# Kernel tuning notes

Measured on AMD Instinct MI355X. Metric: run time of the kernel, lower is better.

The kernel has to match this reference:

```python
import jax, jax.numpy as jnp
import numpy as np

N = 50000      # nodes
E = 800000     # edges (avg degree 16)
IN_DIM = 128
H = 4          # attention heads
D = 32         # hidden dim per head
NEG_SLOPE = 0.2


def setup_inputs() -> dict:
    key = jax.random.key(0)
    ks = jax.random.split(key, 9)
    x = jax.random.normal(ks[0], (N, IN_DIM), dtype=jnp.float32)
    src = jax.random.randint(ks[1], (E,), 0, N, dtype=jnp.int64)
    dst = jax.random.randint(ks[2], (E,), 0, N, dtype=jnp.int64)
    # layer 0: IN_DIM -> H*D ; layer 1: H*D -> H*D
    s0 = 1.0 / np.sqrt(IN_DIM)
    s1 = 1.0 / np.sqrt(H * D)
    W1 = jax.random.normal(ks[3], (H * D, IN_DIM), dtype=jnp.float32) * s0
    al1 = jax.random.normal(ks[4], (1, H, D), dtype=jnp.float32) * s1
    ar1 = jax.random.normal(ks[5], (1, H, D), dtype=jnp.float32) * s1
    W2 = jax.random.normal(ks[6], (H * D, H * D), dtype=jnp.float32) * s1
    al2 = jax.random.normal(ks[7], (1, H, D), dtype=jnp.float32) * s1
    ar2 = jax.random.normal(ks[8], (1, H, D), dtype=jnp.float32) * s1
    return {"x": x, "src": src, "dst": dst, "W1": W1, "al1": al1, "ar1": ar1,
            "W2": W2, "al2": al2, "ar2": ar2}


def gat_conv(h, src, dst, W, al, ar):
    """DGL-style GATConv. h: [N, F_in] -> [N, H, D], with ELU activation."""
    feat = (h @ W.T).reshape(N, H, D)                 # [N,H,D]
    el = jnp.sum(feat * al, axis=-1)                  # [N,H] a_l . Wh
    er = jnp.sum(feat * ar, axis=-1)                  # [N,H] a_r . Wh
    e = jax.nn.leaky_relu(el[src] + er[dst], NEG_SLOPE)  # [E,H]
    # numerically stable edge softmax over incoming edges of each dst node
    m = jax.ops.segment_max(e, dst, num_segments=N)   # [N,H]
    ee = jnp.exp(e - m[dst])                          # [E,H]
    denom = jax.ops.segment_sum(ee, dst, num_segments=N)  # [N,H]
    alpha = ee / denom[dst]                           # [E,H]
    msg = feat[src] * alpha[..., None]                # [E,H,D]
    out = jax.ops.segment_sum(msg, dst, num_segments=N)   # [N,H,D]
    return jax.nn.elu(out)


def reference(x, src, dst, W1, al1, ar1, W2, al2, ar2):
    h = gat_conv(x, src, dst, W1, al1, ar1).reshape(N, H * D)  # flatten(1)
    h = gat_conv(h, src, dst, W2, al2, ar2)                    # [N,H,D]
    return jnp.mean(h, axis=1)                                 # [N,D]
```

## Files before the change

### kernel.cpp

```cpp
#include <hip/hip_runtime.h>
#include <cmath>

#define HEADS 4
#define FDIM 128
#define NEG 0.2f

typedef __attribute__((ext_vector_type(8))) __bf16 bf16x8;
typedef __attribute__((ext_vector_type(8))) _Float16 h16x8;
typedef __attribute__((ext_vector_type(4))) float f32x4;

__global__ __launch_bounds__(256) void prep_kernel(
    const float* __restrict__ W1, const float* __restrict__ al1,
    const float* __restrict__ ar1,
    const float* __restrict__ W2, const float* __restrict__ al2,
    const float* __restrict__ ar2,
    __bf16* __restrict__ wf1, __bf16* __restrict__ wext1,
    __bf16* __restrict__ wf2, __bf16* __restrict__ wext2)
{
    const int b = blockIdx.x, tid = threadIdx.x;
    if (b < 256) {
        const float* W = (b < 128) ? W1 : W2;
        __bf16* wf = (b < 128) ? wf1 : wf2;
        int idx = (b & 127) * 256 + tid;
        int j = idx & 7;
        int r = idx >> 3;
        int c = r & 15; r >>= 4;
        int t = r & 7;  r >>= 3;
        int kq = r & 15;
        int hl = r >> 4;
        float v = W[(t * 16 + c) * 128 + kq * 8 + j];
        __bf16 hi = (__bf16)v;
        wf[idx] = (hl == 0) ? hi : (__bf16)(v - (float)hi);
    } else {
        const float* W  = (b == 256) ? W1 : W2;
        const float* al = (b == 256) ? al1 : al2;
        const float* ar = (b == 256) ? ar1 : ar2;
        __bf16* wext = (b == 256) ? wext1 : wext2;
        __shared__ float val[1024];
        #pragma unroll
        for (int ch = 0; ch < 4; ++ch) {
            int idx = ch * 256 + tid;
            int c = idx >> 7, k = idx & 127;
            int h = c & 3;
            const float* a = (c < 4) ? al : ar;
            float s = 0.f;
            for (int d = 0; d < 32; ++d)
                s += a[h * 32 + d] * W[(h * 32 + d) * 128 + k];
            val[c * 128 + k] = s;
        }
        __syncthreads();
        #pragma unroll
        for (int ch = 0; ch < 16; ++ch) {
            int idx = tid * 16 + ch;
            int j = idx & 7;
            int r = idx >> 3;
            int c = r & 15; r >>= 4;
            int kq = r & 15;
            int hl = r >> 4;
            float v = (c < 8) ? val[c * 128 + kq * 8 + j] : 0.f;
            __bf16 hi = (__bf16)v;
            wext[idx] = (hl == 0) ? hi : (__bf16)(v - (float)hi);
        }
    }
}

__global__ __launch_bounds__(256) void gemm_mfma_kernel(
    const float* __restrict__ X, const bf16x8* __restrict__ wf,
    const bf16x8* __restrict__ wext,
    _Float16* __restrict__ featH,
    float* __restrict__ el, float* __restrict__ er,
    int nnodes, int ntiles)
{
    __shared__ bf16x8 lw[4096];
    const int tid = threadIdx.x;
    for (int i = tid; i < 4096; i += 256) lw[i] = wf[i];
    __syncthreads();

    const int wave = tid >> 6, lane = tid & 63;
    const int l15 = lane & 15, quad = lane >> 4;

    int tile = blockIdx.x;
    float4 xr[8], xn[8];

    auto loadX = [&](int tl, float4* dst) {
        int nodeA = tl * 64 + wave * 16 + l15;
        bool v = nodeA < nnodes;
        const float4* xp = (const float4*)(X + (size_t)nodeA * 128);
        #pragma unroll
        for (int ks = 0; ks < 4; ++ks) {
            dst[2 * ks]     = v ? xp[ks * 8 + quad * 2]     : make_float4(0.f, 0.f, 0.f, 0.f);
            dst[2 * ks + 1] = v ? xp[ks * 8 + quad * 2 + 1] : make_float4(0.f, 0.f, 0.f, 0.f);
        }
    };

    loadX(tile, xr);
    while (true) {
        int next = tile + gridDim.x;
        if (next < ntiles) loadX(next, xn);

        f32x4 acc[9];
        #pragma unroll
        for (int t = 0; t < 9; ++t) acc[t] = (f32x4){0.f, 0.f, 0.f, 0.f};

        #pragma unroll
        for (int ks = 0; ks < 4; ++ks) {
            float xa[8] = {xr[2 * ks].x, xr[2 * ks].y, xr[2 * ks].z, xr[2 * ks].w,
                           xr[2 * ks + 1].x, xr[2 * ks + 1].y, xr[2 * ks + 1].z, xr[2 * ks + 1].w};
            bf16x8 ahi, alo;
            #pragma unroll
            for (int j = 0; j < 8; ++j) {
                __bf16 h = (__bf16)xa[j];
                ahi[j] = h;
                alo[j] = (__bf16)(xa[j] - (float)h);
            }
            const int kq = ks * 4 + quad;

            {
                bf16x8 bh = wext[(kq) * 16 + l15];
                bf16x8 bl = wext[(16 + kq) * 16 + l15];
                acc[8] = __builtin_amdgcn_mfma_f32_16x16x32_bf16(ahi, bh, acc[8], 0, 0, 0);
                acc[8] = __builtin_amdgcn_mfma_f32_16x16x32_bf16(alo, bh, acc[8], 0, 0, 0);
                acc[8] = __builtin_amdgcn_mfma_f32_16x16x32_bf16(ahi, bl, acc[8], 0, 0, 0);
            }
            #pragma unroll
            for (int t = 0; t < 8; ++t) {
                bf16x8 bh = lw[(kq * 8 + t) * 16 + l15];
                bf16x8 bl = lw[((16 + kq) * 8 + t) * 16 + l15];
                acc[t] = __builtin_amdgcn_mfma_f32_16x16x32_bf16(ahi, bh, acc[t], 0, 0, 0);
                acc[t] = __builtin_amdgcn_mfma_f32_16x16x32_bf16(alo, bh, acc[t], 0, 0, 0);
                acc[t] = __builtin_amdgcn_mfma_f32_16x16x32_bf16(ahi, bl, acc[t], 0, 0, 0);
            }
        }

        const int nodeC = tile * 64 + wave * 16 + quad * 4;
        #pragma unroll
        for (int r = 0; r < 4; ++r) {
            int gn = nodeC + r;
            if (gn < nnodes) {
                #pragma unroll
                for (int t = 0; t < 8; ++t)
                    featH[(size_t)gn * 128 + t * 16 + l15] = (_Float16)acc[t][r];
            }
        }
        if (l15 < 8) {
            #pragma unroll
            for (int r = 0; r < 4; ++r) {
                int gn = nodeC + r;
                if (gn < nnodes) {
                    if (l15 < 4) el[gn * HEADS + l15] = acc[8][r];
                    else         er[gn * HEADS + (l15 - 4)] = acc[8][r];
                }
            }
        }

        if (next >= ntiles) break;
        #pragma unroll
        for (int i = 0; i < 8; ++i) xr[i] = xn[i];
        tile = next;
    }
}

__global__ __launch_bounds__(256) void hist_kernel(
    const int* __restrict__ dst, int* __restrict__ counts,
    int* __restrict__ rank, int nedges)
{
    int i0 = (blockIdx.x * 256 + threadIdx.x) * 4;
    if (i0 + 3 < nedges) {
        int4 d = *(const int4*)&dst[i0];
        int4 r;
        r.x = atomicAdd(&counts[d.x], 1);
        r.y = atomicAdd(&counts[d.y], 1);
        r.z = atomicAdd(&counts[d.z], 1);
        r.w = atomicAdd(&counts[d.w], 1);
        *(int4*)&rank[i0] = r;
    } else {
        for (int i = i0; i < nedges; ++i)
            rank[i] = atomicAdd(&counts[dst[i]], 1);
    }
}

__global__ __launch_bounds__(256) void scan1_kernel(
    const int* __restrict__ counts, int* __restrict__ offsets,
    int* __restrict__ bsums, int n)
{
    __shared__ int wsums[4];
    const int tid = threadIdx.x, lane = tid & 63, w = tid >> 6;
    const int i = blockIdx.x * 1024 + tid * 4;

    int4 v = make_int4(0, 0, 0, 0);
    if (i + 3 < n) v = *(const int4*)&counts[i];
    else {
        if (i < n)     v.x = counts[i];
        if (i + 1 < n) v.y = counts[i + 1];
        if (i + 2 < n) v.z = counts[i + 2];
    }
    int s0 = v.x, s1 = s0 + v.y, s2 = s1 + v.z, s3 = s2 + v.w;

    int x = s3;
    #pragma unroll
    for (int off = 1; off < 64; off <<= 1) {
        int t = __shfl_up(x, off, 64);
        if (lane >= off) x += t;
    }
    if (lane == 63) wsums[w] = x;
    __syncthreads();
    int wbase = 0;
    #pragma unroll
    for (int k = 0; k < 4; ++k) if (k < w) wbase += wsums[k];

    int tbase = wbase + x - s3;
    if (i < n)     offsets[i]     = tbase;
    if (i + 1 < n) offsets[i + 1] = tbase + s0;
    if (i + 2 < n) offsets[i + 2] = tbase + s1;
    if (i + 3 < n) offsets[i + 3] = tbase + s2;
    if (tid == 255) bsums[blockIdx.x] = wbase + x;
}

__global__ __launch_bounds__(64) void scan2_kernel(int* __restrict__ bsums, int nb)
{
    const int lane = threadIdx.x;
    int run = 0;
    for (int base = 0; base < nb; base += 64) {
        int i = base + lane;
        int v = (i < nb) ? bsums[i] : 0;
        int x = v;
        #pragma unroll
        for (int off = 1; off < 64; off <<= 1) {
            int t = __shfl_up(x, off, 64);
            if (lane >= off) x += t;
        }
        if (i < nb) bsums[i] = run + x - v;
        run += __shfl(x, 63, 64);
    }
}

__global__ __launch_bounds__(256) void scan3_kernel(
    int* __restrict__ offsets, const int* __restrict__ bsums, int n, int nedges)
{
    const int i = blockIdx.x * 1024 + threadIdx.x * 4;
    const int base = bsums[blockIdx.x];
    #pragma unroll
    for (int k = 0; k < 4; ++k)
        if (i + k < n) offsets[i + k] += base;
    if (blockIdx.x == 0 && threadIdx.x == 0) offsets[n] = nedges;
}

__global__ __launch_bounds__(256) void scatter_kernel(
    const int* __restrict__ src, const int* __restrict__ dst,
    const int* __restrict__ rank, const int* __restrict__ offsets,
    int* __restrict__ csr_src, int nedges)
{
    int i0 = (blockIdx.x * 256 + threadIdx.x) * 4;
    if (i0 + 3 < nedges) {
        int4 d = *(const int4*)&dst[i0];
        int4 r = *(const int4*)&rank[i0];
        int4 s = *(const int4*)&src[i0];
        csr_src[offsets[d.x] + r.x] = s.x;
        csr_src[offsets[d.y] + r.y] = s.y;
        csr_src[offsets[d.z] + r.z] = s.z;
        csr_src[offsets[d.w] + r.w] = s.w;
    } else {
        for (int i = i0; i < nedges; ++i)
            csr_src[offsets[dst[i]] + rank[i]] = src[i];
    }
}

template <bool MEAN>
__global__ __launch_bounds__(256) void aggregate_kernel(
    const _Float16* __restrict__ featH, const float* __restrict__ el,
    const float* __restrict__ er, const int* __restrict__ offsets,
    const int* __restrict__ csr_src, float* __restrict__ out, int nnodes)
{
    const int wid = (blockIdx.x * 256 + threadIdx.x) >> 6;
    const int lane = threadIdx.x & 63;
    const int g = lane >> 4, u = lane & 15, h = u >> 2;
    const int n = wid * 4 + g;
    const bool nv = n < nnodes;

    int beg = 0, end = 0;
    float ern = 0.f;
    if (nv) {
        beg = offsets[n];
        end = offsets[n + 1];
        ern = er[n * HEADS + h];
    }
    int md = end - beg;
    md = max(md, __shfl_xor(md, 16, 64));
    md = max(md, __shfl_xor(md, 32, 64));

    float a[8];
    #pragma unroll
    for (int p = 0; p < 8; ++p) a[p] = 0.f;
    float sw = 0.f;

    int j = beg;
    bool v = j < end;
    int s = v ? csr_src[j] : 0;
    float q = el[s * HEADS + h];
    h16x8 f = ((const h16x8*)(featH + (size_t)s * 128))[u];

    for (int it = 0; it < md; ++it) {
        int jn = j + 1;
        bool vn = jn < end;
        int sn = vn ? csr_src[jn] : 0;
        float qn = el[sn * HEADS + h];
        h16x8 fn = ((const h16x8*)(featH + (size_t)sn * 128))[u];

        float e = q + ern;
        e = e > 0.f ? e : NEG * e;
        float w = v ? __expf(e) : 0.f;
        #pragma unroll
        for (int p = 0; p < 8; ++p) a[p] += w * (float)f[p];
        sw += w;

        j = jn; v = vn; q = qn; f = fn;
    }

    float inv = sw > 0.f ? 1.f / sw : 0.f;
    float r[8];
    #pragma unroll
    for (int p = 0; p < 8; ++p) {
        float t = a[p] * inv;
        r[p] = t > 0.f ? t : expm1f(t);
    }

    if (!MEAN) {
        if (nv) {
            float4* o4 = (float4*)(out + (size_t)n * 128 + u * 8);
            o4[0] = make_float4(r[0], r[1], r[2], r[3]);
            o4[1] = make_float4(r[4], r[5], r[6], r[7]);
        }
    } else {
        #pragma unroll
        for (int p = 0; p < 8; ++p) {
            r[p] += __shfl_xor(r[p], 4, 64);
            r[p] += __shfl_xor(r[p], 8, 64);
        }
        if (nv && u < 4) {
            float4* o4 = (float4*)(out + (size_t)n * 32 + u * 8);
            o4[0] = make_float4(0.25f * r[0], 0.25f * r[1], 0.25f * r[2], 0.25f * r[3]);
            o4[1] = make_float4(0.25f * r[4], 0.25f * r[5], 0.25f * r[6], 0.25f * r[7]);
        }
    }
}

extern "C" void kernel_launch(void* const* d_in, const int* in_sizes, int n_in,
                              void* d_out, int out_size, void* d_ws, size_t ws_size,
                              hipStream_t stream)
{
    const float* x   = (const float*)d_in[0];
    const int*   src = (const int*)d_in[1];
    const int*   dst = (const int*)d_in[2];
    const float* W1  = (const float*)d_in[3];
    const float* al1 = (const float*)d_in[4];
    const float* ar1 = (const float*)d_in[5];
    const float* W2  = (const float*)d_in[6];
    const float* al2 = (const float*)d_in[7];
    const float* ar2 = (const float*)d_in[8];
    float* out = (float*)d_out;

    const int N = in_sizes[0] / FDIM;
    const int E = in_sizes[1];

    float* h1 = (float*)d_ws;
    _Float16* featH = (_Float16*)(h1 + (size_t)N * FDIM);
    float* el = (float*)(featH + (size_t)N * FDIM);
    float* er = el + (size_t)N * HEADS;
    int* counts  = (int*)(er + (size_t)N * HEADS);
    int* offsets = counts + N;
    int* rank    = offsets + (N + 1);
    int* csr_src = rank + E;
    int* bsums   = csr_src + E;
    uintptr_t wp = ((uintptr_t)(bsums + 256) + 63) & ~(uintptr_t)63;
    __bf16* wf1   = (__bf16*)wp;
    __bf16* wext1 = wf1 + 32768;
    __bf16* wf2   = wext1 + 4096;
    __bf16* wext2 = wf2 + 32768;

    const int ntiles = (N + 63) / 64;
    const int gemm_grid = ntiles < 512 ? ntiles : 512;
    const int edge4_grid = ((E + 3) / 4 + 255) / 256;
    const int agg_grid  = ((N + 3) / 4 + 3) / 4;
    const int nscan     = (N + 1023) / 1024;

    prep_kernel<<<258, 256, 0, stream>>>(W1, al1, ar1, W2, al2, ar2,
                                         wf1, wext1, wf2, wext2);

    hipMemsetAsync(counts, 0, (size_t)N * sizeof(int), stream);
    hist_kernel<<<edge4_grid, 256, 0, stream>>>(dst, counts, rank, E);
    scan1_kernel<<<nscan, 256, 0, stream>>>(counts, offsets, bsums, N);
    scan2_kernel<<<1, 64, 0, stream>>>(bsums, nscan);
    scan3_kernel<<<nscan, 256, 0, stream>>>(offsets, bsums, N, E);
    scatter_kernel<<<edge4_grid, 256, 0, stream>>>(src, dst, rank, offsets, csr_src, E);

    gemm_mfma_kernel<<<gemm_grid, 256, 0, stream>>>(
        x, (const bf16x8*)wf1, (const bf16x8*)wext1, featH, el, er, N, ntiles);
    aggregate_kernel<false><<<agg_grid, 256, 0, stream>>>(
        featH, el, er, offsets, csr_src, h1, N);

    gemm_mfma_kernel<<<gemm_grid, 256, 0, stream>>>(
        h1, (const bf16x8*)wf2, (const bf16x8*)wext2, featH, el, er, N, ntiles);
    aggregate_kernel<true><<<agg_grid, 256, 0, stream>>>(
        featH, el, er, offsets, csr_src, out, N);
}
```

Measured before the change: 257.9 us.

## Sort CSR neighbors by source bucket, store layer-1 output in fp16, halve GEMM grid

Each destination's incoming edges are split into 8 buckets by source index range, so the aggregation gathers feature rows in roughly increasing address order. The intermediate h1 is stored as fp16 instead of fp32, and the second GEMM is templated to read fp16 input, halving that traffic. The GEMM grid is capped at 256 blocks instead of 512. In exchange the counts/offsets arrays and the scan grow eightfold, and h1 loses precision to fp16 rounding.

Result: faster. 250.0 us (-3.0%).

```diff
diff --git a/kernel.cpp b/kernel.cpp
--- a/kernel.cpp
+++ b/kernel.cpp
@@ -1,9 +1,11 @@
 #include <hip/hip_runtime.h>
 #include <cmath>
+#include <type_traits>
 
 #define HEADS 4
 #define FDIM 128
 #define NEG 0.2f
+#define NBUCK 8
 
 typedef __attribute__((ext_vector_type(8))) __bf16 bf16x8;
 typedef __attribute__((ext_vector_type(8))) _Float16 h16x8;
@@ -64,8 +66,9 @@
     }
 }
 
+template <typename XT>
 __global__ __launch_bounds__(256) void gemm_mfma_kernel(
-    const float* __restrict__ X, const bf16x8* __restrict__ wf,
+    const XT* __restrict__ X, const bf16x8* __restrict__ wf,
     const bf16x8* __restrict__ wext,
     _Float16* __restrict__ featH,
     float* __restrict__ el, float* __restrict__ er,
@@ -80,16 +83,36 @@
     const int l15 = lane & 15, quad = lane >> 4;
 
     int tile = blockIdx.x;
-    float4 xr[8], xn[8];
-
-    auto loadX = [&](int tl, float4* dst) {
+    float xr[32], xn[32];
+
+    auto loadX = [&](int tl, float* dst) {
         int nodeA = tl * 64 + wave * 16 + l15;
         bool v = nodeA < nnodes;
-        const float4* xp = (const float4*)(X + (size_t)nodeA * 128);
-        #pragma unroll
-        for (int ks = 0; ks < 4; ++ks) {
-            dst[2 * ks]     = v ? xp[ks * 8 + quad * 2]     : make_float4(0.f, 0.f, 0.f, 0.f);
-            dst[2 * ks + 1] = v ? xp[ks * 8 + quad * 2 + 1] : make_float4(0.f, 0.f, 0.f, 0.f);
+        if constexpr (std::is_same<XT, float>::value) {
+            const float4* xp = (const float4*)(X + (size_t)nodeA * 128);
+            #pragma unroll
+            for (int ks = 0; ks < 4; ++ks) {
+                float4 a = v ? xp[ks * 8 + quad * 2]     : make_float4(0.f, 0.f, 0.f, 0.f);
+                float4 b = v ? xp[ks * 8 + quad * 2 + 1] : make_float4(0.f, 0.f, 0.f, 0.f);
+                dst[ks * 8 + 0] = a.x; dst[ks * 8 + 1] = a.y;
+                dst[ks * 8 + 2] = a.z; dst[ks * 8 + 3] = a.w;
+                dst[ks * 8 + 4] = b.x; dst[ks * 8 + 5] = b.y;
+                dst[ks * 8 + 6] = b.z; dst[ks * 8 + 7] = b.w;
+            }
+        } else {
+            const h16x8* xp = (const h16x8*)(X + (size_t)nodeA * 128);
+            #pragma unroll
+            for (int ks = 0; ks < 4; ++ks) {
+                h16x8 hv;
+                if (v) {
+                    hv = xp[ks * 4 + quad];
+                } else {
+                    #pragma unroll
+                    for (int j = 0; j < 8; ++j) hv[j] = (_Float16)0.f;
+                }
+                #pragma unroll
+                for (int j = 0; j < 8; ++j) dst[ks * 8 + j] = (float)hv[j];
+            }
         }
     };
 
@@ -104,14 +127,13 @@
 
         #pragma unroll
         for (int ks = 0; ks < 4; ++ks) {
-            float xa[8] = {xr[2 * ks].x, xr[2 * ks].y, xr[2 * ks].z, xr[2 * ks].w,
-                           xr[2 * ks + 1].x, xr[2 * ks + 1].y, xr[2 * ks + 1].z, xr[2 * ks + 1].w};
             bf16x8 ahi, alo;
             #pragma unroll
             for (int j = 0; j < 8; ++j) {
-                __bf16 h = (__bf16)xa[j];
+                float xv = xr[ks * 8 + j];
+                __bf16 h = (__bf16)xv;
                 ahi[j] = h;
-                alo[j] = (__bf16)(xa[j] - (float)h);
+                alo[j] = (__bf16)(xv - (float)h);
             }
             const int kq = ks * 4 + quad;
 
@@ -155,27 +177,28 @@
 
         if (next >= ntiles) break;
         #pragma unroll
-        for (int i = 0; i < 8; ++i) xr[i] = xn[i];
+        for (int i = 0; i < 32; ++i) xr[i] = xn[i];
         tile = next;
     }
 }
 
 __global__ __launch_bounds__(256) void hist_kernel(
-    const int* __restrict__ dst, int* __restrict__ counts,
-    int* __restrict__ rank, int nedges)
+    const int* __restrict__ src, const int* __restrict__ dst,
+    int* __restrict__ counts, int* __restrict__ rank, int nedges, int shift)
 {
     int i0 = (blockIdx.x * 256 + threadIdx.x) * 4;
     if (i0 + 3 < nedges) {
         int4 d = *(const int4*)&dst[i0];
+        int4 s = *(const int4*)&src[i0];
         int4 r;
-        r.x = atomicAdd(&counts[d.x], 1);
-        r.y = atomicAdd(&counts[d.y], 1);
-        r.z = atomicAdd(&counts[d.z], 1);
-        r.w = atomicAdd(&counts[d.w], 1);
+        r.x = atomicAdd(&counts[d.x * NBUCK + (s.x >> shift)], 1);
+        r.y = atomicAdd(&counts[d.y * NBUCK + (s.y >> shift)], 1);
+        r.z = atomicAdd(&counts[d.z * NBUCK + (s.z >> shift)], 1);
+        r.w = atomicAdd(&counts[d.w * NBUCK + (s.w >> shift)], 1);
         *(int4*)&rank[i0] = r;
     } else {
         for (int i = i0; i < nedges; ++i)
-            rank[i] = atomicAdd(&counts[dst[i]], 1);
+            rank[i] = atomicAdd(&counts[dst[i] * NBUCK + (src[i] >> shift)], 1);
     }
 }
 
@@ -248,20 +271,20 @@
 __global__ __launch_bounds__(256) void scatter_kernel(
     const int* __restrict__ src, const int* __restrict__ dst,
     const int* __restrict__ rank, const int* __restrict__ offsets,
-    int* __restrict__ csr_src, int nedges)
+    int* __restrict__ csr_src, int nedges, int shift)
 {
     int i0 = (blockIdx.x * 256 + threadIdx.x) * 4;
     if (i0 + 3 < nedges) {
         int4 d = *(const int4*)&dst[i0];
         int4 r = *(const int4*)&rank[i0];
         int4 s = *(const int4*)&src[i0];
-        csr_src[offsets[d.x] + r.x] = s.x;
-        csr_src[offsets[d.y] + r.y] = s.y;
-        csr_src[offsets[d.z] + r.z] = s.z;
-        csr_src[offsets[d.w] + r.w] = s.w;
+        csr_src[offsets[d.x * NBUCK + (s.x >> shift)] + r.x] = s.x;
+        csr_src[offsets[d.y * NBUCK + (s.y >> shift)] + r.y] = s.y;
+        csr_src[offsets[d.z * NBUCK + (s.z >> shift)] + r.z] = s.z;
+        csr_src[offsets[d.w * NBUCK + (s.w >> shift)] + r.w] = s.w;
     } else {
         for (int i = i0; i < nedges; ++i)
-            csr_src[offsets[dst[i]] + rank[i]] = src[i];
+            csr_src[offsets[dst[i] * NBUCK + (src[i] >> shift)] + rank[i]] = src[i];
     }
 }
 
@@ -269,7 +292,7 @@
 __global__ __launch_bounds__(256) void aggregate_kernel(
     const _Float16* __restrict__ featH, const float* __restrict__ el,
     const float* __restrict__ er, const int* __restrict__ offsets,
-    const int* __restrict__ csr_src, float* __restrict__ out, int nnodes)
+    const int* __restrict__ csr_src, void* __restrict__ outp, int nnodes)
 {
     const int wid = (blockIdx.x * 256 + threadIdx.x) >> 6;
     const int lane = threadIdx.x & 63;
@@ -280,8 +303,8 @@
     int beg = 0, end = 0;
     float ern = 0.f;
     if (nv) {
-        beg = offsets[n];
-        end = offsets[n + 1];
+        beg = offsets[n * NBUCK];
+        end = offsets[n * NBUCK + NBUCK];
         ern = er[n * HEADS + h];
     }
     int md = end - beg;
@@ -326,9 +349,10 @@
 
     if (!MEAN) {
         if (nv) {
-            float4* o4 = (float4*)(out + (size_t)n * 128 + u * 8);
-            o4[0] = make_float4(r[0], r[1], r[2], r[3]);
-            o4[1] = make_float4(r[4], r[5], r[6], r[7]);
+            h16x8 o;
+            #pragma unroll
+            for (int p = 0; p < 8; ++p) o[p] = (_Float16)r[p];
+            ((h16x8*)outp)[(size_t)n * 16 + u] = o;
         }
     } else {
         #pragma unroll
@@ -337,6 +361,7 @@
             r[p] += __shfl_xor(r[p], 8, 64);
         }
         if (nv && u < 4) {
+            float* out = (float*)outp;
             float4* o4 = (float4*)(out + (size_t)n * 32 + u * 8);
             o4[0] = make_float4(0.25f * r[0], 0.25f * r[1], 0.25f * r[2], 0.25f * r[3]);
             o4[1] = make_float4(0.25f * r[4], 0.25f * r[5], 0.25f * r[6], 0.25f * r[7]);
@@ -357,49 +382,53 @@
     const float* W2  = (const float*)d_in[6];
     const float* al2 = (const float*)d_in[7];
     const float* ar2 = (const float*)d_in[8];
-    float* out = (float*)d_out;
 
     const int N = in_sizes[0] / FDIM;
     const int E = in_sizes[1];
-
-    float* h1 = (float*)d_ws;
-    _Float16* featH = (_Float16*)(h1 + (size_t)N * FDIM);
+    const int NB = N * NBUCK;
+
+    int shift = 0;
+    while (((N - 1) >> shift) > (NBUCK - 1)) ++shift;
+
+    _Float16* h1 = (_Float16*)d_ws;
+    _Float16* featH = h1 + (size_t)N * FDIM;
     float* el = (float*)(featH + (size_t)N * FDIM);
     float* er = el + (size_t)N * HEADS;
     int* counts  = (int*)(er + (size_t)N * HEADS);
-    int* offsets = counts + N;
-    int* rank    = offsets + (N + 1);
+    int* offsets = counts + NB;
+    int* rank    = offsets + (NB + 1);
     int* csr_src = rank + E;
     int* bsums   = csr_src + E;
-    uintptr_t wp = ((uintptr_t)(bsums + 256) + 63) & ~(uintptr_t)63;
+    uintptr_t wp = ((uintptr_t)(bsums + 512) + 63) & ~(uintptr_t)63;
     __bf16* wf1   = (__bf16*)wp;
     __bf16* wext1 = wf1 + 32768;
     __bf16* wf2   = wext1 + 4096;
     __bf16* wext2 = wf2 + 32768;
 
     const int ntiles = (N + 63) / 64;
-    const int gemm_grid = ntiles < 512 ? ntiles : 512;
+    const int gemm_grid = ntiles < 256 ? ntiles : 256;
     const int edge4_grid = ((E + 3) / 4 + 255) / 256;
     const int agg_grid  = ((N + 3) / 4 + 3) / 4;
-    const int nscan     = (N + 1023) / 1024;
+    const int nscan     = (NB + 1023) / 1024;
 
     prep_kernel<<<258, 256, 0, stream>>>(W1, al1, ar1, W2, al2, ar2,
                                          wf1, wext1, wf2, wext2);
 
-    hipMemsetAsync(counts, 0, (size_t)N * sizeof(int), stream);
-    hist_kernel<<<edge4_grid, 256, 0, stream>>>(dst, counts, rank, E);
-    scan1_kernel<<<nscan, 256, 0, stream>>>(counts, offsets, bsums, N);
+    (void)hipMemsetAsync(counts, 0, (size_t)NB * sizeof(int), stream);
+    hist_kernel<<<edge4_grid, 256, 0, stream>>>(src, dst, counts, rank, E, shift);
+    scan1_kernel<<<nscan, 256, 0, stream>>>(counts, offsets, bsums, NB);
     scan2_kernel<<<1, 64, 0, stream>>>(bsums, nscan);
-    scan3_kernel<<<nscan, 256, 0, stream>>>(offsets, bsums, N, E);
-    scatter_kernel<<<edge4_grid, 256, 0, stream>>>(src, dst, rank, offsets, csr_src, E);
-
-    gemm_mfma_kernel<<<gemm_grid, 256, 0, stream>>>(
+    scan3_kernel<<<nscan, 256, 0, stream>>>(offsets, bsums, NB, E);
+    scatter_kernel<<<edge4_grid, 256, 0, stream>>>(src, dst, rank, offsets,
+                                                   csr_src, E, shift);
+
+    gemm_mfma_kernel<float><<<gemm_grid, 256, 0, stream>>>(
         x, (const bf16x8*)wf1, (const bf16x8*)wext1, featH, el, er, N, ntiles);
     aggregate_kernel<false><<<agg_grid, 256, 0, stream>>>(
-        featH, el, er, offsets, csr_src, h1, N);
-
-    gemm_mfma_kernel<<<gemm_grid, 256, 0, stream>>>(
+        featH, el, er, offsets, csr_src, (void*)h1, N);
+
+    gemm_mfma_kernel<_Float16><<<gemm_grid, 256, 0, stream>>>(
         h1, (const bf16x8*)wf2, (const bf16x8*)wext2, featH, el, er, N, ntiles);
     aggregate_kernel<true><<<agg_grid, 256, 0, stream>>>(
-        featH, el, er, offsets, csr_src, out, N);
-}
+        featH, el, er, offsets, csr_src, d_out, N);
+}
```
